# Optimization experiments

Hardware: AMD Instinct MI355X
Metric: run time of the kernel (lower is better)

The kernel has to match this reference:

```python
import jax, jax.numpy as jnp
import numpy as np

PI = float(np.pi)
B, N_ATOMS = 512, 512            # batch, atoms in backbone chain
N_DIST, N_ANG, N_DIH = N_ATOMS - 1, N_ATOMS - 2, N_ATOMS - 3
LEFT_SPLIT, RIGHT_SPLIT = 255, 254  # split-1 and N-split-2 with split = N_ATOMS//2


def setup_inputs() -> dict:
    key = jax.random.key(0)
    k1, k2, k3 = jax.random.split(key, 3)
    # bond lengths ~ [1.0, 1.5) Angstrom-ish, bond angles in (0.5, 2.5) rad,
    # dihedrals in [-pi, pi) -- scaled uniforms so the chain is non-degenerate.
    distances = 1.0 + 0.5 * jax.random.uniform(k1, (B, N_DIST), dtype=jnp.float32)
    angles = 0.5 + 2.0 * jax.random.uniform(k2, (B, N_ANG), dtype=jnp.float32)
    dihedrals = 2.0 * PI * jax.random.uniform(k3, (B, N_DIH), dtype=jnp.float32) - PI
    return {"distances": distances, "angles": angles, "dihedrals": dihedrals,
            "left_split": LEFT_SPLIT, "right_split": RIGHT_SPLIT}


def _alt_sign(n, dtype):
    # +1, -1, +1, ... of length n
    return 1.0 - 2.0 * (jnp.arange(n) % 2).astype(dtype)


def rotation_matrix(axis, angle):
    """Rodrigues rotation matrices. axis: (B,3) unit vectors, angle: (B,) -> (B,3,3)."""
    c = jnp.cos(angle)[:, None, None]
    s = jnp.sin(angle)[:, None, None]
    ax, ay, az = axis[:, 0], axis[:, 1], axis[:, 2]
    z = jnp.zeros_like(ax)
    K = jnp.stack([jnp.stack([z, -az, ay], axis=-1),
                   jnp.stack([az, z, -ax], axis=-1),
                   jnp.stack([-ay, ax, z], axis=-1)], axis=1)  # (B,3,3) cross-product matrix
    outer = axis[:, :, None] * axis[:, None, :]
    return c * jnp.eye(3, dtype=axis.dtype) + s * K + (1.0 - c) * outer


def chain_in_plane(lengths, angles):
    """Vectorized form of encodermap.chain_in_plane.
    lengths: (1, n_len), angles: (B, n_len-1) -> cartesians (B, n_len+1, 3) in the z=0 plane.
    prev_angle recurrence a_i = pi - angles_i - a_{i-1} solved in closed form via signed cumsum."""
    dt = angles.dtype
    Bb, n_ang = angles.shape
    n_len = lengths.shape[1]
    sa = _alt_sign(n_ang, dt)                       # (-1)^k
    a = sa * jnp.cumsum(sa * (PI - angles), axis=1)  # prev_angle after step i, (B, n_ang)
    theta = jnp.concatenate([jnp.zeros((Bb, 1), dt), a], axis=1)  # segment headings, (B, n_len)
    sign = _alt_sign(n_len, dt)
    dx = lengths * jnp.cos(theta)                    # broadcast (1,n_len)*(B,n_len)
    dy = lengths * jnp.sin(theta) * sign
    xs = jnp.concatenate([jnp.zeros((Bb, 1), dt), jnp.cumsum(dx, axis=1)], axis=1)
    ys = jnp.concatenate([jnp.zeros((Bb, 1), dt), jnp.cumsum(dy, axis=1)], axis=1)
    return jnp.stack([xs, ys, jnp.zeros_like(xs)], axis=2)


def dihedral_to_cartesian_one_way(dihedrals, cart, n):
    """Sequential rebuild: at step i rotate the tail (points >= i+2 of rotated) about the
    bond (i -> i+1) by -dihedral_i. Fixed-shape lax.scan carry with an index mask replaces
    the original's shrinking concat, computing identical values."""
    dih = -dihedrals[:, :n]                 # (B, n)
    r0 = cart[:, 1:]                        # (B, L-1, 3)
    idx = jnp.arange(r0.shape[1])

    def step(r, xs):
        i, d = xs
        prev = jnp.take(r, i, axis=1)       # (B,3)
        off = jnp.take(r, i + 1, axis=1)    # (B,3)
        axis = off - prev
        axis = axis / jnp.linalg.norm(axis, axis=1, keepdims=True)
        R = rotation_matrix(axis, d)        # (B,3,3)
        rot = off[:, None, :] + jnp.einsum('bnd,bde->bne', r - off[:, None, :], R)
        mask = (idx >= i + 2)[None, :, None]
        return jnp.where(mask, rot, r), None

    rF, _ = jax.lax.scan(step, r0, (jnp.arange(n), jnp.swapaxes(dih, 0, 1)))
    return jnp.concatenate([cart[:, :1], rF], axis=1)  # (B, L, 3)


def backmap(distances, angles, dihedrals, left_split, right_split):
    # mean bond lengths over batch, shape (1, n_len)
    lengths = jnp.mean(distances, axis=0, keepdims=True)
    cart = chain_in_plane(lengths, angles)          # (B, N, 3)
    dih = dihedrals + PI
    N = cart.shape[1]
    split = N // 2
    cart_r = cart[:, split - 1:]                    # (B, N-split+1, 3)
    dih_r = dih[:, split - 1:]
    cart_l = jnp.flip(cart[:, :split + 2], axis=1)  # cart[:, split+1::-1]
    dih_l = jnp.flip(dih[:, :split - 1], axis=1)    # dih[:, split-2::-1]
    new_r = dihedral_to_cartesian_one_way(dih_r, cart_r, right_split)
    new_l = dihedral_to_cartesian_one_way(dih_l, cart_l, left_split)
    return jnp.concatenate([jnp.flip(new_l, axis=1), new_r[:, 3:]], axis=1)  # (B, N, 3)


def reference(distances, angles, dihedrals, left_split, right_split):
    return backmap(distances, angles, dihedrals, left_split, right_split)
```

## Files before the change

### kernel.cpp

```cpp
#include <hip/hip_runtime.h>
#include <math.h>

namespace {
constexpr int kB = 512;
constexpr int kNDist = 511;
constexpr int kNAng = 510;
constexpr int kNDih = 509;
constexpr int kNPt = 512;
constexpr float kPi = 3.14159265358979323846f;
}

__global__ void k_lengths(const float* __restrict__ dist, float* __restrict__ len) {
  __shared__ float red[256];
  const int j = blockIdx.x;
  const int t = threadIdx.x;
  float s = dist[(size_t)t * kNDist + j] + dist[(size_t)(t + 256) * kNDist + j];
  red[t] = s;
  __syncthreads();
#pragma unroll
  for (int off = 128; off > 0; off >>= 1) {
    if (t < off) red[t] += red[t + off];
    __syncthreads();
  }
  if (t == 0) len[j] = red[0] * (1.0f / 512.0f);
}

__global__ __launch_bounds__(512) void k_backmap(
    const float* __restrict__ angles,
    const float* __restrict__ dih,
    const float* __restrict__ len,
    float* __restrict__ out) {
  const int b = blockIdx.x;
  const int tid = threadIdx.x;

  __shared__ float s_len[kNPt];
  __shared__ float s_f[kNPt];
  __shared__ float2 s_f2[kNPt];
  __shared__ float s_cx[kNPt];
  __shared__ float s_cy[kNPt];
  __shared__ float s_m[2][256][9];
  __shared__ float s_v[2][256][3];

  if (tid < kNDist) s_len[tid] = len[tid];

  float t0 = 0.f;
  if (tid < kNAng) {
    const float sa = (tid & 1) ? -1.f : 1.f;
    t0 = sa * (kPi - angles[(size_t)b * kNAng + tid]);
  }
  float v = t0;
  s_f[tid] = v;
  __syncthreads();
#pragma unroll
  for (int off = 1; off < kNPt; off <<= 1) {
    float add = (tid >= off) ? s_f[tid - off] : 0.f;
    __syncthreads();
    v += add;
    s_f[tid] = v;
    __syncthreads();
  }
  float theta = 0.f;
  if (tid >= 1 && tid < kNDist) {
    const float sa = ((tid - 1) & 1) ? -1.f : 1.f;
    theta = sa * s_f[tid - 1];
  }
  float dxv = 0.f, dyv = 0.f;
  if (tid < kNDist) {
    float sn, cs;
    sincosf(theta, &sn, &cs);
    const float L = s_len[tid];
    const float sg = (tid & 1) ? -1.f : 1.f;
    dxv = L * cs;
    dyv = L * sn * sg;
  }
  float2 v2 = make_float2(dxv, dyv);
  s_f2[tid] = v2;
  __syncthreads();
#pragma unroll
  for (int off = 1; off < kNPt; off <<= 1) {
    float ax = 0.f, ay = 0.f;
    if (tid >= off) { float2 w = s_f2[tid - off]; ax = w.x; ay = w.y; }
    __syncthreads();
    v2.x += ax; v2.y += ay;
    s_f2[tid] = v2;
    __syncthreads();
  }
  float px = 0.f, py = 0.f;
  if (tid >= 1) { float2 w = s_f2[tid - 1]; px = w.x; py = w.y; }
  s_cx[tid] = px;
  s_cy[tid] = py;
  __syncthreads();

  const int side = tid >> 8;
  const int k = tid & 255;
  const int nb = side ? 255 : 256;
  const int ng = side ? 254 : 255;

  float bx = 0.f, by = 0.f;
  if (k < nb) {
    const int i0 = side ? (256 + k) : (256 - k);
    const int i1 = side ? (257 + k) : (255 - k);
    bx = s_cx[i1] - s_cx[i0];
    by = s_cy[i1] - s_cy[i0];
  }

  float m0 = 1.f, m1 = 0.f, m2 = 0.f, m3 = 0.f, m4 = 1.f, m5 = 0.f,
        m6 = 0.f, m7 = 0.f, m8 = 1.f;
  if (k < ng) {
    const float phi = side ? (dih[(size_t)b * kNDih + 255 + k] + kPi)
                           : (dih[(size_t)b * kNDih + 254 - k] + kPi);
    const float rn = rsqrtf(bx * bx + by * by);
    const float ax = bx * rn, ay = by * rn;
    float sp, cp;
    sincosf(phi, &sp, &cp);
    const float omc = 1.f - cp;
    m0 = cp + omc * ax * ax;  m1 = omc * ax * ay;      m2 = sp * ay;
    m3 = omc * ax * ay;       m4 = cp + omc * ay * ay; m5 = -sp * ax;
    m6 = -sp * ay;            m7 = sp * ax;            m8 = cp;
  }
  {
    float* M = s_m[side][k];
    M[0]=m0; M[1]=m1; M[2]=m2; M[3]=m3; M[4]=m4; M[5]=m5; M[6]=m6; M[7]=m7; M[8]=m8;
  }
  __syncthreads();
#pragma unroll
  for (int off = 1; off < 256; off <<= 1) {
    float n0=0,n1=0,n2=0,n3=0,n4=0,n5=0,n6=0,n7=0,n8=0;
    const bool has = (k >= off);
    if (has) {
      const float* N = s_m[side][k - off];
      n0=N[0]; n1=N[1]; n2=N[2]; n3=N[3]; n4=N[4]; n5=N[5]; n6=N[6]; n7=N[7]; n8=N[8];
    }
    __syncthreads();
    if (has) {
      const float a0 = n0*m0 + n1*m3 + n2*m6;
      const float a1 = n0*m1 + n1*m4 + n2*m7;
      const float a2 = n0*m2 + n1*m5 + n2*m8;
      const float a3 = n3*m0 + n4*m3 + n5*m6;
      const float a4 = n3*m1 + n4*m4 + n5*m7;
      const float a5 = n3*m2 + n4*m5 + n5*m8;
      const float a6 = n6*m0 + n7*m3 + n8*m6;
      const float a7 = n6*m1 + n7*m4 + n8*m7;
      const float a8 = n6*m2 + n7*m5 + n8*m8;
      m0=a0; m1=a1; m2=a2; m3=a3; m4=a4; m5=a5; m6=a6; m7=a7; m8=a8;
    }
    float* M = s_m[side][k];
    M[0]=m0; M[1]=m1; M[2]=m2; M[3]=m3; M[4]=m4; M[5]=m5; M[6]=m6; M[7]=m7; M[8]=m8;
    __syncthreads();
  }

  float cx = 0.f, cy = 0.f, cz = 0.f;
  if (k < nb) {
    if (k == 0) {
      cx = bx; cy = by; cz = 0.f;
    } else {
      const float* S = s_m[side][k - 1];
      cx = S[0]*bx + S[1]*by;
      cy = S[3]*bx + S[4]*by;
      cz = S[6]*bx + S[7]*by;
    }
  }
  float vx = cx, vy = cy, vz = cz;
  {
    float* V = s_v[side][k];
    V[0]=vx; V[1]=vy; V[2]=vz;
  }
  __syncthreads();
#pragma unroll
  for (int off = 1; off < 256; off <<= 1) {
    float ax=0.f, ay=0.f, az=0.f;
    if (k >= off) {
      const float* W = s_v[side][k - off];
      ax=W[0]; ay=W[1]; az=W[2];
    }
    __syncthreads();
    vx+=ax; vy+=ay; vz+=az;
    float* V = s_v[side][k];
    V[0]=vx; V[1]=vy; V[2]=vz;
    __syncthreads();
  }

  const float bpx = s_cx[256], bpy = s_cy[256];
  const float ox = bpx + vx, oy = bpy + vy, oz = vz;
  float* outb = out + (size_t)b * 512 * 3;
  if (side == 0) {
    const int row = 255 - k;
    outb[row*3+0] = ox; outb[row*3+1] = oy; outb[row*3+2] = oz;
  } else {
    if (k >= 1 && k <= 254) {
      const int row = 257 + k;
      outb[row*3+0] = ox; outb[row*3+1] = oy; outb[row*3+2] = oz;
    }
    if (k == 0) {
      outb[256*3+0] = bpx; outb[256*3+1] = bpy; outb[256*3+2] = 0.f;
    }
    if (k == 255) {
      outb[257*3+0] = s_cx[257]; outb[257*3+1] = s_cy[257]; outb[257*3+2] = 0.f;
    }
  }
}

extern "C" void kernel_launch(void* const* d_in, const int* in_sizes, int n_in,
                              void* d_out, int out_size, void* d_ws, size_t ws_size,
                              hipStream_t stream) {
  const float* distances = (const float*)d_in[0];
  const float* angles    = (const float*)d_in[1];
  const float* dihedrals = (const float*)d_in[2];
  float* lengths = (float*)d_ws;
  float* out = (float*)d_out;
  k_lengths<<<kNDist, 256, 0, stream>>>(distances, lengths);
  k_backmap<<<kB, 512, 0, stream>>>(angles, dihedrals, lengths, out);
}
```

Before: 76.64 us.

## Use wave-shuffle scans and quaternion composition; coalesce length reduction with atomics

All block-level prefix scans move from shared-memory Hillis-Steele loops with two barriers per step to 64-lane shuffle scans, followed by a small cross-wave combine through shared memory. The 3x3 rotation-matrix product scan becomes a quaternion scan, which carries fewer values per shuffle and needs fewer multiplies per composition. The per-column mean-length kernel now reads distance rows coalesced and accumulates into the output with atomics after a memset. In exchange, the float atomic adds make the summation order nondeterministic, quaternion composition rounds differently from the matrix path, and there is one extra memset launch.

```diff
diff --git a/kernel.cpp b/kernel.cpp
--- a/kernel.cpp
+++ b/kernel.cpp
@@ -6,23 +6,26 @@
 constexpr int kNDist = 511;
 constexpr int kNAng = 510;
 constexpr int kNDih = 509;
-constexpr int kNPt = 512;
 constexpr float kPi = 3.14159265358979323846f;
 }
 
-__global__ void k_lengths(const float* __restrict__ dist, float* __restrict__ len) {
-  __shared__ float red[256];
-  const int j = blockIdx.x;
+__device__ __forceinline__ float shflu(float v, int off) {
+  return __shfl_up(v, off, 64);
+}
+
+__global__ __launch_bounds__(256) void k_lengths(const float* __restrict__ dist,
+                                                 float* __restrict__ len) {
   const int t = threadIdx.x;
-  float s = dist[(size_t)t * kNDist + j] + dist[(size_t)(t + 256) * kNDist + j];
-  red[t] = s;
-  __syncthreads();
-#pragma unroll
-  for (int off = 128; off > 0; off >>= 1) {
-    if (t < off) red[t] += red[t + off];
-    __syncthreads();
-  }
-  if (t == 0) len[j] = red[0] * (1.0f / 512.0f);
+  const int r0 = blockIdx.x * 4;
+  float a0 = 0.f, a1 = 0.f;
+#pragma unroll
+  for (int r = 0; r < 4; ++r) {
+    const float* row = dist + (size_t)(r0 + r) * kNDist;
+    a0 += row[t];
+    if (t < kNDist - 256) a1 += row[t + 256];
+  }
+  atomicAdd(&len[t], a0 * (1.0f / 512.0f));
+  if (t < kNDist - 256) atomicAdd(&len[t + 256], a1 * (1.0f / 512.0f));
 }
 
 __global__ __launch_bounds__(512) void k_backmap(
@@ -32,67 +35,71 @@
     float* __restrict__ out) {
   const int b = blockIdx.x;
   const int tid = threadIdx.x;
-
-  __shared__ float s_len[kNPt];
-  __shared__ float s_f[kNPt];
-  __shared__ float2 s_f2[kNPt];
-  __shared__ float s_cx[kNPt];
-  __shared__ float s_cy[kNPt];
-  __shared__ float s_m[2][256][9];
-  __shared__ float s_v[2][256][3];
-
-  if (tid < kNDist) s_len[tid] = len[tid];
+  const int wave = tid >> 6;
+  const int lane = tid & 63;
+
+  __shared__ float s_cx[512];
+  __shared__ float s_cy[512];
+  __shared__ float s_ws1[8];
+  __shared__ float s_ws2[8][2];
+  __shared__ float s_wq[2][4][4];
+  __shared__ float s_wv[2][4][3];
 
   float t0 = 0.f;
   if (tid < kNAng) {
     const float sa = (tid & 1) ? -1.f : 1.f;
     t0 = sa * (kPi - angles[(size_t)b * kNAng + tid]);
   }
-  float v = t0;
-  s_f[tid] = v;
-  __syncthreads();
-#pragma unroll
-  for (int off = 1; off < kNPt; off <<= 1) {
-    float add = (tid >= off) ? s_f[tid - off] : 0.f;
-    __syncthreads();
-    v += add;
-    s_f[tid] = v;
-    __syncthreads();
-  }
+  float iv = t0;
+#pragma unroll
+  for (int off = 1; off < 64; off <<= 1) {
+    float w = shflu(iv, off);
+    if (lane >= off) iv += w;
+  }
+  if (lane == 63) s_ws1[wave] = iv;
+  __syncthreads();
+  float p = 0.f;
+  for (int j = 0; j < wave; ++j) p += s_ws1[j];
+  float full = iv + p;
+  float prevScan = shflu(full, 1);
+  if (lane == 0) prevScan = p;
+
   float theta = 0.f;
   if (tid >= 1 && tid < kNDist) {
     const float sa = ((tid - 1) & 1) ? -1.f : 1.f;
-    theta = sa * s_f[tid - 1];
-  }
+    theta = sa * prevScan;
+  }
+
   float dxv = 0.f, dyv = 0.f;
   if (tid < kNDist) {
     float sn, cs;
     sincosf(theta, &sn, &cs);
-    const float L = s_len[tid];
+    const float L = len[tid];
     const float sg = (tid & 1) ? -1.f : 1.f;
     dxv = L * cs;
     dyv = L * sn * sg;
   }
-  float2 v2 = make_float2(dxv, dyv);
-  s_f2[tid] = v2;
-  __syncthreads();
-#pragma unroll
-  for (int off = 1; off < kNPt; off <<= 1) {
-    float ax = 0.f, ay = 0.f;
-    if (tid >= off) { float2 w = s_f2[tid - off]; ax = w.x; ay = w.y; }
-    __syncthreads();
-    v2.x += ax; v2.y += ay;
-    s_f2[tid] = v2;
-    __syncthreads();
-  }
+  float ix = dxv, iy = dyv;
+#pragma unroll
+  for (int off = 1; off < 64; off <<= 1) {
+    float wx = shflu(ix, off);
+    float wy = shflu(iy, off);
+    if (lane >= off) { ix += wx; iy += wy; }
+  }
+  if (lane == 63) { s_ws2[wave][0] = ix; s_ws2[wave][1] = iy; }
+  __syncthreads();
   float px = 0.f, py = 0.f;
-  if (tid >= 1) { float2 w = s_f2[tid - 1]; px = w.x; py = w.y; }
-  s_cx[tid] = px;
-  s_cy[tid] = py;
+  for (int j = 0; j < wave; ++j) { px += s_ws2[j][0]; py += s_ws2[j][1]; }
+  float fx = ix + px, fy = iy + py;
+  float cxe = shflu(fx, 1), cye = shflu(fy, 1);
+  if (lane == 0) { cxe = px; cye = py; }
+  s_cx[tid] = cxe;
+  s_cy[tid] = cye;
   __syncthreads();
 
   const int side = tid >> 8;
   const int k = tid & 255;
+  const int swave = (tid >> 6) & 3;
   const int nb = side ? 255 : 256;
   const int ng = side ? 254 : 255;
 
@@ -104,98 +111,93 @@
     by = s_cy[i1] - s_cy[i0];
   }
 
-  float m0 = 1.f, m1 = 0.f, m2 = 0.f, m3 = 0.f, m4 = 1.f, m5 = 0.f,
-        m6 = 0.f, m7 = 0.f, m8 = 1.f;
+  float qw = 1.f, qx = 0.f, qy = 0.f, qz = 0.f;
   if (k < ng) {
     const float phi = side ? (dih[(size_t)b * kNDih + 255 + k] + kPi)
                            : (dih[(size_t)b * kNDih + 254 - k] + kPi);
     const float rn = rsqrtf(bx * bx + by * by);
-    const float ax = bx * rn, ay = by * rn;
-    float sp, cp;
-    sincosf(phi, &sp, &cp);
-    const float omc = 1.f - cp;
-    m0 = cp + omc * ax * ax;  m1 = omc * ax * ay;      m2 = sp * ay;
-    m3 = omc * ax * ay;       m4 = cp + omc * ay * ay; m5 = -sp * ax;
-    m6 = -sp * ay;            m7 = sp * ax;            m8 = cp;
-  }
-  {
-    float* M = s_m[side][k];
-    M[0]=m0; M[1]=m1; M[2]=m2; M[3]=m3; M[4]=m4; M[5]=m5; M[6]=m6; M[7]=m7; M[8]=m8;
-  }
-  __syncthreads();
-#pragma unroll
-  for (int off = 1; off < 256; off <<= 1) {
-    float n0=0,n1=0,n2=0,n3=0,n4=0,n5=0,n6=0,n7=0,n8=0;
-    const bool has = (k >= off);
-    if (has) {
-      const float* N = s_m[side][k - off];
-      n0=N[0]; n1=N[1]; n2=N[2]; n3=N[3]; n4=N[4]; n5=N[5]; n6=N[6]; n7=N[7]; n8=N[8];
-    }
-    __syncthreads();
-    if (has) {
-      const float a0 = n0*m0 + n1*m3 + n2*m6;
-      const float a1 = n0*m1 + n1*m4 + n2*m7;
-      const float a2 = n0*m2 + n1*m5 + n2*m8;
-      const float a3 = n3*m0 + n4*m3 + n5*m6;
-      const float a4 = n3*m1 + n4*m4 + n5*m7;
-      const float a5 = n3*m2 + n4*m5 + n5*m8;
-      const float a6 = n6*m0 + n7*m3 + n8*m6;
-      const float a7 = n6*m1 + n7*m4 + n8*m7;
-      const float a8 = n6*m2 + n7*m5 + n8*m8;
-      m0=a0; m1=a1; m2=a2; m3=a3; m4=a4; m5=a5; m6=a6; m7=a7; m8=a8;
-    }
-    float* M = s_m[side][k];
-    M[0]=m0; M[1]=m1; M[2]=m2; M[3]=m3; M[4]=m4; M[5]=m5; M[6]=m6; M[7]=m7; M[8]=m8;
-    __syncthreads();
-  }
-
-  float cx = 0.f, cy = 0.f, cz = 0.f;
-  if (k < nb) {
-    if (k == 0) {
-      cx = bx; cy = by; cz = 0.f;
-    } else {
-      const float* S = s_m[side][k - 1];
-      cx = S[0]*bx + S[1]*by;
-      cy = S[3]*bx + S[4]*by;
-      cz = S[6]*bx + S[7]*by;
-    }
-  }
+    float sh, ch;
+    sincosf(0.5f * phi, &sh, &ch);
+    qw = ch;
+    qx = sh * bx * rn;
+    qy = sh * by * rn;
+  }
+#pragma unroll
+  for (int off = 1; off < 64; off <<= 1) {
+    float aw = shflu(qw, off), ax = shflu(qx, off),
+          ay = shflu(qy, off), az = shflu(qz, off);
+    if (lane >= off) {
+      const float nw = aw * qw - ax * qx - ay * qy - az * qz;
+      const float nx = aw * qx + ax * qw + ay * qz - az * qy;
+      const float ny = aw * qy - ax * qz + ay * qw + az * qx;
+      const float nz = aw * qz + ax * qy - ay * qx + az * qw;
+      qw = nw; qx = nx; qy = ny; qz = nz;
+    }
+  }
+  if (lane == 63) {
+    float* W = s_wq[side][swave];
+    W[0] = qw; W[1] = qx; W[2] = qy; W[3] = qz;
+  }
+  __syncthreads();
+  float Pw = 1.f, Px = 0.f, Py = 0.f, Pz = 0.f;
+  for (int j = 0; j < swave; ++j) {
+    const float* W = s_wq[side][j];
+    const float aw = Pw, ax = Px, ay = Py, az = Pz;
+    const float bw = W[0], bxq = W[1], byq = W[2], bzq = W[3];
+    Pw = aw * bw - ax * bxq - ay * byq - az * bzq;
+    Px = aw * bxq + ax * bw + ay * bzq - az * byq;
+    Py = aw * byq - ax * bzq + ay * bw + az * bxq;
+    Pz = aw * bzq + ax * byq - ay * bxq + az * bw;
+  }
+  float Qw = Pw * qw - Px * qx - Py * qy - Pz * qz;
+  float Qx = Pw * qx + Px * qw + Py * qz - Pz * qy;
+  float Qy = Pw * qy - Px * qz + Py * qw + Pz * qx;
+  float Qz = Pw * qz + Px * qy - Py * qx + Pz * qw;
+  float Ww = shflu(Qw, 1), Wx = shflu(Qx, 1), Wy = shflu(Qy, 1), Wz = shflu(Qz, 1);
+  if (lane == 0) { Ww = Pw; Wx = Px; Wy = Py; Wz = Pz; }
+
+  const float tx = -2.f * Wz * by;
+  const float ty = 2.f * Wz * bx;
+  const float tz = 2.f * (Wx * by - Wy * bx);
+  float cx = bx + Ww * tx + (Wy * tz - Wz * ty);
+  float cy = by + Ww * ty + (Wz * tx - Wx * tz);
+  float cz = Ww * tz + (Wx * ty - Wy * tx);
+
   float vx = cx, vy = cy, vz = cz;
-  {
-    float* V = s_v[side][k];
-    V[0]=vx; V[1]=vy; V[2]=vz;
-  }
-  __syncthreads();
-#pragma unroll
-  for (int off = 1; off < 256; off <<= 1) {
-    float ax=0.f, ay=0.f, az=0.f;
-    if (k >= off) {
-      const float* W = s_v[side][k - off];
-      ax=W[0]; ay=W[1]; az=W[2];
-    }
-    __syncthreads();
-    vx+=ax; vy+=ay; vz+=az;
-    float* V = s_v[side][k];
-    V[0]=vx; V[1]=vy; V[2]=vz;
-    __syncthreads();
-  }
+#pragma unroll
+  for (int off = 1; off < 64; off <<= 1) {
+    float ax = shflu(vx, off), ay = shflu(vy, off), az = shflu(vz, off);
+    if (lane >= off) { vx += ax; vy += ay; vz += az; }
+  }
+  if (lane == 63) {
+    float* V = s_wv[side][swave];
+    V[0] = vx; V[1] = vy; V[2] = vz;
+  }
+  __syncthreads();
+  float sx = 0.f, sy = 0.f, sz = 0.f;
+  for (int j = 0; j < swave; ++j) {
+    const float* V = s_wv[side][j];
+    sx += V[0]; sy += V[1]; sz += V[2];
+  }
+  vx += sx; vy += sy; vz += sz;
 
   const float bpx = s_cx[256], bpy = s_cy[256];
   const float ox = bpx + vx, oy = bpy + vy, oz = vz;
   float* outb = out + (size_t)b * 512 * 3;
   if (side == 0) {
     const int row = 255 - k;
-    outb[row*3+0] = ox; outb[row*3+1] = oy; outb[row*3+2] = oz;
+    outb[row * 3 + 0] = ox; outb[row * 3 + 1] = oy; outb[row * 3 + 2] = oz;
   } else {
     if (k >= 1 && k <= 254) {
       const int row = 257 + k;
-      outb[row*3+0] = ox; outb[row*3+1] = oy; outb[row*3+2] = oz;
+      outb[row * 3 + 0] = ox; outb[row * 3 + 1] = oy; outb[row * 3 + 2] = oz;
     }
     if (k == 0) {
-      outb[256*3+0] = bpx; outb[256*3+1] = bpy; outb[256*3+2] = 0.f;
+      outb[256 * 3 + 0] = bpx; outb[256 * 3 + 1] = bpy; outb[256 * 3 + 2] = 0.f;
     }
     if (k == 255) {
-      outb[257*3+0] = s_cx[257]; outb[257*3+1] = s_cy[257]; outb[257*3+2] = 0.f;
+      outb[257 * 3 + 0] = s_cx[257]; outb[257 * 3 + 1] = s_cy[257];
+      outb[257 * 3 + 2] = 0.f;
     }
   }
 }
@@ -208,6 +210,7 @@
   const float* dihedrals = (const float*)d_in[2];
   float* lengths = (float*)d_ws;
   float* out = (float*)d_out;
-  k_lengths<<<kNDist, 256, 0, stream>>>(distances, lengths);
+  hipMemsetAsync(lengths, 0, kNDist * sizeof(float), stream);
+  k_lengths<<<kB / 4, 256, 0, stream>>>(distances, lengths);
   k_backmap<<<kB, 512, 0, stream>>>(angles, dihedrals, lengths, out);
 }
```

New measurement: 76.88 us. Within noise of the previous version (+0.3%).
